# Performance work log

Hardware: AMD Instinct MI355X
Metric: run time of the kernel (lower is better)

Reference implementation:

```python
import jax, jax.numpy as jnp
import numpy as np

B, N, S, K = 8, 16384, 1024, 32
C_STEM, C_PATCH, PE_DIM = 64, 128, 24
RADIUS = 0.2
NUM_BANDS = PE_DIM // 6  # 4 freq bands, sin+cos per xyz axis -> 3*2*4 = 24


def setup_inputs() -> dict:
    key = jax.random.key(0)
    ks = jax.random.split(key, 6)
    xyz = jax.random.uniform(ks[0], (B, N, 3), dtype=jnp.float32)
    point_feature = jax.random.normal(ks[1], (B, N, C_STEM), dtype=jnp.float32)
    patch_center = jax.random.uniform(ks[2], (B, S, 3), dtype=jnp.float32)
    in_dim = C_STEM + 3 + PE_DIM  # grouped_feature + relative_xyz + pos-enc
    w1 = jax.random.normal(ks[3], (in_dim, C_PATCH), dtype=jnp.float32) / np.sqrt(in_dim)
    b1 = jnp.zeros((C_PATCH,), dtype=jnp.float32)
    w2 = jax.random.normal(ks[4], (C_PATCH, C_PATCH), dtype=jnp.float32) / np.sqrt(C_PATCH)
    b2 = jnp.zeros((C_PATCH,), dtype=jnp.float32)
    return dict(xyz=xyz, point_feature=point_feature, patch_center=patch_center,
                w1=w1, b1=b1, w2=w2, b2=b2)


def query_ball_point(radius, nsample, xyz, new_xyz):
    # Standard PointNet++ ball query. xyz:[B,N,3], new_xyz:[B,S,3] -> idx:[B,S,K]
    n = xyz.shape[1]
    sqrdists = jnp.sum((new_xyz[:, :, None, :] - xyz[:, None, :, :]) ** 2, axis=-1)  # [B,S,N]
    gi = jnp.where(sqrdists > radius * radius, n,
                   jnp.arange(n, dtype=jnp.int32)[None, None, :])
    gi = jnp.sort(gi, axis=-1)[:, :, :nsample]           # first K in-ball indices
    first = gi[:, :, :1]
    gi = jnp.where(gi == n, first, gi)                   # pad misses with first hit
    return jnp.minimum(gi, n - 1)


def index_points(points, idx):
    # points:[B,N,C], idx:[B,S,K] -> [B,S,K,C]
    b = points.shape[0]
    return points[jnp.arange(b)[:, None, None], idx]


def pos_encode(rel):
    # NeRF-style sinusoidal encoding of relative xyz: [...,3] -> [...,PE_DIM]
    freqs = (2.0 ** jnp.arange(NUM_BANDS, dtype=jnp.float32)) * jnp.pi
    ang = rel[..., None] * freqs                          # [...,3,NB]
    enc = jnp.concatenate([jnp.sin(ang), jnp.cos(ang)], axis=-1)  # [...,3,2NB]
    return enc.reshape(rel.shape[:-1] + (PE_DIM,))


def reference(xyz, point_feature, patch_center, w1, b1, w2, b2):
    neighbor_idx = query_ball_point(RADIUS, K, xyz, patch_center)   # [B,S,K]
    grouped_xyz = index_points(xyz, neighbor_idx)                    # [B,S,K,3]
    grouped_feature = index_points(point_feature, neighbor_idx)      # [B,S,K,C_STEM]
    relative_xyz = grouped_xyz - patch_center[:, :, None, :]
    relative_position = pos_encode(relative_xyz)                     # [B,S,K,PE_DIM]
    grouped_input = jnp.concatenate(
        (grouped_feature, relative_xyz, relative_position), axis=-1)  # [B,S,K,91]
    h = jax.nn.relu(grouped_input @ w1 + b1)   # PointMLP 1 (shared per-point MLP)
    h = h @ w2 + b2                            # PointMLP 2 (no activation)
    patch_feature = jnp.max(h, axis=2)         # max-pool over K neighbors -> [B,S,C_PATCH]
    return (patch_feature, neighbor_idx)
```

## Files before the change

kernel.cpp:

```cpp
#include <hip/hip_runtime.h>
#include <hip/hip_bf16.h>

#define B_ 8
#define N_ 16384
#define S_ 1024
#define K_ 32
#define CSTEM 64
#define CPATCH 128
#define INDIM 91
#define LDA 104
#define LDH 136

typedef __attribute__((ext_vector_type(8))) short short8v;
typedef __attribute__((ext_vector_type(4))) float f32x4;

static __device__ __forceinline__ unsigned short f2bf(float f) {
  union { float f; unsigned int u; } v; v.f = f;
  return (unsigned short)((v.u + 0x7FFFu + ((v.u >> 16) & 1u)) >> 16);
}

__global__ __launch_bounds__(256) void pack_weights(
    const float* __restrict__ w1, const float* __restrict__ w2,
    unsigned short* __restrict__ w1p, unsigned short* __restrict__ w2p)
{
  const int id = blockIdx.x * 256 + threadIdx.x;
  if (id < 3 * 8 * 64) {
    const int l = id & 63, ct = (id >> 6) & 7, ks = id >> 9;
    const int col = 16 * ct + (l & 15);
    const int kb = 32 * ks + (l >> 4) * 8;
    unsigned short v[8];
    #pragma unroll
    for (int j = 0; j < 8; ++j) {
      const int k = kb + j;
      v[j] = (k < INDIM) ? f2bf(w1[k * CPATCH + col]) : (unsigned short)0;
    }
    *(short8v*)&w1p[(size_t)id * 8] = *(const short8v*)v;
  } else if (id < 3 * 8 * 64 + 4 * 8 * 64) {
    const int id2 = id - 3 * 8 * 64;
    const int l = id2 & 63, ct = (id2 >> 6) & 7, ks = id2 >> 9;
    const int col = 16 * ct + (l & 15);
    const int kb = 32 * ks + (l >> 4) * 8;
    unsigned short v[8];
    #pragma unroll
    for (int j = 0; j < 8; ++j) v[j] = f2bf(w2[(kb + j) * CPATCH + col]);
    *(short8v*)&w2p[(size_t)id2 * 8] = *(const short8v*)v;
  }
}

__global__ __launch_bounds__(256, 6) void ball_query_kernel(
    const float* __restrict__ xyz, const float* __restrict__ pc,
    float* __restrict__ idx_out)
{
  const int w    = threadIdx.x >> 6;
  const int lane = threadIdx.x & 63;
  const int bs   = blockIdx.x * 4 + w;
  const int b    = bs >> 10;

  const float* __restrict__ xb = xyz + (size_t)b * N_ * 3;
  const double cx = (double)pc[bs * 3 + 0];
  const double cy = (double)pc[bs * 3 + 1];
  const double cz = (double)pc[bs * 3 + 2];
  const double rr = 0.2 * 0.2;

  __shared__ int fidx[4][K_];

  const unsigned long long lower = (1ull << lane) - 1ull;
  int found = 0;
  for (int base = 0; base < N_; base += 256) {
    const int i0 = base + lane * 4;
    const float4 p0 = *(const float4*)&xb[i0 * 3 + 0];
    const float4 p1 = *(const float4*)&xb[i0 * 3 + 4];
    const float4 p2 = *(const float4*)&xb[i0 * 3 + 8];

    double dx, dy, dz;
    dx = (double)p0.x - cx; dy = (double)p0.y - cy; dz = (double)p0.z - cz;
    const bool in0 = (dx * dx + dy * dy + dz * dz) <= rr;
    dx = (double)p0.w - cx; dy = (double)p1.x - cy; dz = (double)p1.y - cz;
    const bool in1 = (dx * dx + dy * dy + dz * dz) <= rr;
    dx = (double)p1.z - cx; dy = (double)p1.w - cy; dz = (double)p2.x - cz;
    const bool in2 = (dx * dx + dy * dy + dz * dz) <= rr;
    dx = (double)p2.y - cx; dy = (double)p2.z - cy; dz = (double)p2.w - cz;
    const bool in3 = (dx * dx + dy * dy + dz * dz) <= rr;

    const unsigned long long b0 = __ballot(in0);
    const unsigned long long b1 = __ballot(in1);
    const unsigned long long b2 = __ballot(in2);
    const unsigned long long b3 = __ballot(in3);

    int p = found + __popcll(b0 & lower) + __popcll(b1 & lower)
                  + __popcll(b2 & lower) + __popcll(b3 & lower);
    if (in0) { if (p < K_) fidx[w][p] = i0 + 0; ++p; }
    if (in1) { if (p < K_) fidx[w][p] = i0 + 1; ++p; }
    if (in2) { if (p < K_) fidx[w][p] = i0 + 2; ++p; }
    if (in3) { if (p < K_) fidx[w][p] = i0 + 3; }

    found += __popcll(b0) + __popcll(b1) + __popcll(b2) + __popcll(b3);
    if (found >= K_) break;
  }
  __threadfence_block();
  if (lane < K_) {
    const int fill = (found == 0) ? (N_ - 1) : fidx[w][0];
    const int v = (lane < found) ? fidx[w][lane] : fill;
    idx_out[(size_t)bs * K_ + lane] = (float)v;
  }
}

__global__ __launch_bounds__(256) void patch_mlp_mfma(
    const float* __restrict__ xyz, const float* __restrict__ pf,
    const float* __restrict__ pc,
    const unsigned short* __restrict__ w1p, const float* __restrict__ b1,
    const unsigned short* __restrict__ w2p, const float* __restrict__ b2,
    const float* __restrict__ idx_f, float* __restrict__ out)
{
  const int bs   = blockIdx.x;
  const int b    = bs >> 10;
  const int tid  = threadIdx.x;
  const int lane = tid & 63;
  const int w    = tid >> 6;

  __shared__ int sidx[K_];
  __shared__ float scen[3];
  __shared__ __align__(16) unsigned short As[K_][LDA];
  __shared__ __align__(16) unsigned short Hs[K_][LDH];

  if (tid < K_) sidx[tid] = (int)idx_f[(size_t)bs * K_ + tid];
  if (tid < 3)  scen[tid] = pc[bs * 3 + tid];
  __syncthreads();

  const float* __restrict__ pfb = pf  + (size_t)b * N_ * CSTEM;
  const float* __restrict__ xb  = xyz + (size_t)b * N_ * 3;

  {
    const int row = tid >> 3, sub = tid & 7;
    const int r = sidx[row];
    const float4 f0 = *(const float4*)&pfb[(size_t)r * CSTEM + sub * 8];
    const float4 f1 = *(const float4*)&pfb[(size_t)r * CSTEM + sub * 8 + 4];
    unsigned short v[8];
    v[0] = f2bf(f0.x); v[1] = f2bf(f0.y); v[2] = f2bf(f0.z); v[3] = f2bf(f0.w);
    v[4] = f2bf(f1.x); v[5] = f2bf(f1.y); v[6] = f2bf(f1.z); v[7] = f2bf(f1.w);
    *(short8v*)&As[row][sub * 8] = *(const short8v*)v;
  }
  {
    const int row = tid & 31, j = tid >> 5;
    const int r = sidx[row];
    float rel[3];
    rel[0] = xb[r * 3 + 0] - scen[0];
    rel[1] = xb[r * 3 + 1] - scen[1];
    rel[2] = xb[r * 3 + 2] - scen[2];
    #pragma unroll
    for (int cc = 0; cc < 4; ++cc) {
      const int c = 64 + 4 * j + cc;
      float val;
      if (c < 67) val = rel[c - 64];
      else if (c < 91) {
        const int q = c - 67, d = q >> 3, rbit = q & 7, band = rbit & 3;
        const float ang = rel[d] * ((float)(1 << band) * 3.14159265358979323846f);
        val = (rbit < 4) ? sinf(ang) : cosf(ang);
      } else val = 0.f;
      As[row][c] = f2bf(val);
    }
  }
  __syncthreads();

  f32x4 acc[2][2] = {};
  #pragma unroll
  for (int ks = 0; ks < 3; ++ks) {
    const int k0 = ks * 32 + (lane >> 4) * 8;
    const short8v a0 = *(const short8v*)&As[(lane & 15)][k0];
    const short8v a1 = *(const short8v*)&As[16 + (lane & 15)][k0];
    const short8v bA = *(const short8v*)&w1p[((size_t)(ks * 8 + 2 * w) * 64 + lane) * 8];
    const short8v bB = *(const short8v*)&w1p[((size_t)(ks * 8 + 2 * w + 1) * 64 + lane) * 8];
    acc[0][0] = __builtin_amdgcn_mfma_f32_16x16x32_bf16(a0, bA, acc[0][0], 0, 0, 0);
    acc[0][1] = __builtin_amdgcn_mfma_f32_16x16x32_bf16(a0, bB, acc[0][1], 0, 0, 0);
    acc[1][0] = __builtin_amdgcn_mfma_f32_16x16x32_bf16(a1, bA, acc[1][0], 0, 0, 0);
    acc[1][1] = __builtin_amdgcn_mfma_f32_16x16x32_bf16(a1, bB, acc[1][1], 0, 0, 0);
  }
  const float bias1[2] = { b1[32 * w + (lane & 15)], b1[32 * w + 16 + (lane & 15)] };
  #pragma unroll
  for (int rt = 0; rt < 2; ++rt)
    #pragma unroll
    for (int t = 0; t < 2; ++t)
      #pragma unroll
      for (int reg = 0; reg < 4; ++reg) {
        const float h = fmaxf(acc[rt][t][reg] + bias1[t], 0.f);
        const int row = 16 * rt + (lane >> 4) * 4 + reg;
        const int col = 32 * w + 16 * t + (lane & 15);
        Hs[row][col] = f2bf(h);
      }
  __syncthreads();

  f32x4 acc2[2][2] = {};
  #pragma unroll
  for (int ks = 0; ks < 4; ++ks) {
    const int k0 = ks * 32 + (lane >> 4) * 8;
    const short8v a0 = *(const short8v*)&Hs[(lane & 15)][k0];
    const short8v a1 = *(const short8v*)&Hs[16 + (lane & 15)][k0];
    const short8v bA = *(const short8v*)&w2p[((size_t)(ks * 8 + 2 * w) * 64 + lane) * 8];
    const short8v bB = *(const short8v*)&w2p[((size_t)(ks * 8 + 2 * w + 1) * 64 + lane) * 8];
    acc2[0][0] = __builtin_amdgcn_mfma_f32_16x16x32_bf16(a0, bA, acc2[0][0], 0, 0, 0);
    acc2[0][1] = __builtin_amdgcn_mfma_f32_16x16x32_bf16(a0, bB, acc2[0][1], 0, 0, 0);
    acc2[1][0] = __builtin_amdgcn_mfma_f32_16x16x32_bf16(a1, bA, acc2[1][0], 0, 0, 0);
    acc2[1][1] = __builtin_amdgcn_mfma_f32_16x16x32_bf16(a1, bB, acc2[1][1], 0, 0, 0);
  }
  float m0 = -3.4e38f, m1 = -3.4e38f;
  #pragma unroll
  for (int rt = 0; rt < 2; ++rt)
    #pragma unroll
    for (int reg = 0; reg < 4; ++reg) {
      m0 = fmaxf(m0, acc2[rt][0][reg]);
      m1 = fmaxf(m1, acc2[rt][1][reg]);
    }
  m0 += b2[32 * w + (lane & 15)];
  m1 += b2[32 * w + 16 + (lane & 15)];
  m0 = fmaxf(m0, __shfl_xor(m0, 16));
  m0 = fmaxf(m0, __shfl_xor(m0, 32));
  m1 = fmaxf(m1, __shfl_xor(m1, 16));
  m1 = fmaxf(m1, __shfl_xor(m1, 32));
  if (lane < 16) {
    out[(size_t)bs * CPATCH + 32 * w + lane]      = m0;
    out[(size_t)bs * CPATCH + 32 * w + 16 + lane] = m1;
  }
}

extern "C" void kernel_launch(void* const* d_in, const int* in_sizes, int n_in,
                              void* d_out, int out_size, void* d_ws, size_t ws_size,
                              hipStream_t stream) {
  const float* xyz = (const float*)d_in[0];
  const float* pf  = (const float*)d_in[1];
  const float* pc  = (const float*)d_in[2];
  const float* w1  = (const float*)d_in[3];
  const float* b1  = (const float*)d_in[4];
  const float* w2  = (const float*)d_in[5];
  const float* b2  = (const float*)d_in[6];

  float* out     = (float*)d_out;
  float* idx_out = out + (size_t)B_ * S_ * CPATCH;

  unsigned short* w1p = (unsigned short*)d_ws;
  unsigned short* w2p = w1p + 96 * 128;

  pack_weights<<<14, 256, 0, stream>>>(w1, w2, w1p, w2p);
  ball_query_kernel<<<B_ * S_ / 4, 256, 0, stream>>>(xyz, pc, idx_out);
  patch_mlp_mfma<<<B_ * S_, 256, 0, stream>>>(xyz, pf, pc, w1p, b1, w2p, b2,
                                              idx_out, out);
}
```

Before: 53.90 us.

## Process several patches per MLP block with register-resident weights; prefetch ball-query points

The MLP kernel now handles four patches per block. Each wave loads its W1/W2 MFMA fragments and biases into registers once and reuses them across all four patches, instead of reloading them from global memory for every patch. The ball-query loop is software-pipelined so the next 256-point chunk of xyz is loaded while the current chunk is tested. In exchange the MLP kernel uses more registers and launches fewer blocks, and each patch iteration still runs serially with block-wide barriers, so there is less latency hiding.

```diff
diff --git a/kernel.cpp b/kernel.cpp
--- a/kernel.cpp
+++ b/kernel.cpp
@@ -10,6 +10,7 @@
 #define INDIM 91
 #define LDA 104
 #define LDH 136
+#define PPB 4
 
 typedef __attribute__((ext_vector_type(8))) short short8v;
 typedef __attribute__((ext_vector_type(4))) float f32x4;
@@ -65,21 +66,30 @@
   __shared__ int fidx[4][K_];
 
   const unsigned long long lower = (1ull << lane) - 1ull;
+  const int lo3 = lane * 12;
   int found = 0;
-  for (int base = 0; base < N_; base += 256) {
+  int base = 0;
+
+  float4 c0 = *(const float4*)&xb[lo3 + 0];
+  float4 c1 = *(const float4*)&xb[lo3 + 4];
+  float4 c2 = *(const float4*)&xb[lo3 + 8];
+
+  for (;;) {
+    const bool last = (base + 256 >= N_);
+    const int pb = last ? base : base + 256;
+    const float4 n0 = *(const float4*)&xb[pb * 3 + lo3 + 0];
+    const float4 n1 = *(const float4*)&xb[pb * 3 + lo3 + 4];
+    const float4 n2 = *(const float4*)&xb[pb * 3 + lo3 + 8];
+
     const int i0 = base + lane * 4;
-    const float4 p0 = *(const float4*)&xb[i0 * 3 + 0];
-    const float4 p1 = *(const float4*)&xb[i0 * 3 + 4];
-    const float4 p2 = *(const float4*)&xb[i0 * 3 + 8];
-
     double dx, dy, dz;
-    dx = (double)p0.x - cx; dy = (double)p0.y - cy; dz = (double)p0.z - cz;
+    dx = (double)c0.x - cx; dy = (double)c0.y - cy; dz = (double)c0.z - cz;
     const bool in0 = (dx * dx + dy * dy + dz * dz) <= rr;
-    dx = (double)p0.w - cx; dy = (double)p1.x - cy; dz = (double)p1.y - cz;
+    dx = (double)c0.w - cx; dy = (double)c1.x - cy; dz = (double)c1.y - cz;
     const bool in1 = (dx * dx + dy * dy + dz * dz) <= rr;
-    dx = (double)p1.z - cx; dy = (double)p1.w - cy; dz = (double)p2.x - cz;
+    dx = (double)c1.z - cx; dy = (double)c1.w - cy; dz = (double)c2.x - cz;
     const bool in2 = (dx * dx + dy * dy + dz * dz) <= rr;
-    dx = (double)p2.y - cx; dy = (double)p2.z - cy; dz = (double)p2.w - cz;
+    dx = (double)c2.y - cx; dy = (double)c2.z - cy; dz = (double)c2.w - cz;
     const bool in3 = (dx * dx + dy * dy + dz * dz) <= rr;
 
     const unsigned long long b0 = __ballot(in0);
@@ -95,7 +105,9 @@
     if (in3) { if (p < K_) fidx[w][p] = i0 + 3; }
 
     found += __popcll(b0) + __popcll(b1) + __popcll(b2) + __popcll(b3);
-    if (found >= K_) break;
+    if (found >= K_ || last) break;
+    base += 256;
+    c0 = n0; c1 = n1; c2 = n2;
   }
   __threadfence_block();
   if (lane < K_) {
@@ -105,15 +117,13 @@
   }
 }
 
-__global__ __launch_bounds__(256) void patch_mlp_mfma(
+__global__ __launch_bounds__(256, 2) void patch_mlp_mfma(
     const float* __restrict__ xyz, const float* __restrict__ pf,
     const float* __restrict__ pc,
     const unsigned short* __restrict__ w1p, const float* __restrict__ b1,
     const unsigned short* __restrict__ w2p, const float* __restrict__ b2,
     const float* __restrict__ idx_f, float* __restrict__ out)
 {
-  const int bs   = blockIdx.x;
-  const int b    = bs >> 10;
   const int tid  = threadIdx.x;
   const int lane = tid & 63;
   const int w    = tid >> 6;
@@ -123,102 +133,117 @@
   __shared__ __align__(16) unsigned short As[K_][LDA];
   __shared__ __align__(16) unsigned short Hs[K_][LDH];
 
-  if (tid < K_) sidx[tid] = (int)idx_f[(size_t)bs * K_ + tid];
-  if (tid < 3)  scen[tid] = pc[bs * 3 + tid];
-  __syncthreads();
-
-  const float* __restrict__ pfb = pf  + (size_t)b * N_ * CSTEM;
-  const float* __restrict__ xb  = xyz + (size_t)b * N_ * 3;
-
-  {
-    const int row = tid >> 3, sub = tid & 7;
-    const int r = sidx[row];
-    const float4 f0 = *(const float4*)&pfb[(size_t)r * CSTEM + sub * 8];
-    const float4 f1 = *(const float4*)&pfb[(size_t)r * CSTEM + sub * 8 + 4];
-    unsigned short v[8];
-    v[0] = f2bf(f0.x); v[1] = f2bf(f0.y); v[2] = f2bf(f0.z); v[3] = f2bf(f0.w);
-    v[4] = f2bf(f1.x); v[5] = f2bf(f1.y); v[6] = f2bf(f1.z); v[7] = f2bf(f1.w);
-    *(short8v*)&As[row][sub * 8] = *(const short8v*)v;
-  }
-  {
-    const int row = tid & 31, j = tid >> 5;
-    const int r = sidx[row];
-    float rel[3];
-    rel[0] = xb[r * 3 + 0] - scen[0];
-    rel[1] = xb[r * 3 + 1] - scen[1];
-    rel[2] = xb[r * 3 + 2] - scen[2];
-    #pragma unroll
-    for (int cc = 0; cc < 4; ++cc) {
-      const int c = 64 + 4 * j + cc;
-      float val;
-      if (c < 67) val = rel[c - 64];
-      else if (c < 91) {
-        const int q = c - 67, d = q >> 3, rbit = q & 7, band = rbit & 3;
-        const float ang = rel[d] * ((float)(1 << band) * 3.14159265358979323846f);
-        val = (rbit < 4) ? sinf(ang) : cosf(ang);
-      } else val = 0.f;
-      As[row][c] = f2bf(val);
-    }
-  }
-  __syncthreads();
-
-  f32x4 acc[2][2] = {};
+  short8v w1f[3][2], w2f[4][2];
   #pragma unroll
-  for (int ks = 0; ks < 3; ++ks) {
-    const int k0 = ks * 32 + (lane >> 4) * 8;
-    const short8v a0 = *(const short8v*)&As[(lane & 15)][k0];
-    const short8v a1 = *(const short8v*)&As[16 + (lane & 15)][k0];
-    const short8v bA = *(const short8v*)&w1p[((size_t)(ks * 8 + 2 * w) * 64 + lane) * 8];
-    const short8v bB = *(const short8v*)&w1p[((size_t)(ks * 8 + 2 * w + 1) * 64 + lane) * 8];
-    acc[0][0] = __builtin_amdgcn_mfma_f32_16x16x32_bf16(a0, bA, acc[0][0], 0, 0, 0);
-    acc[0][1] = __builtin_amdgcn_mfma_f32_16x16x32_bf16(a0, bB, acc[0][1], 0, 0, 0);
-    acc[1][0] = __builtin_amdgcn_mfma_f32_16x16x32_bf16(a1, bA, acc[1][0], 0, 0, 0);
-    acc[1][1] = __builtin_amdgcn_mfma_f32_16x16x32_bf16(a1, bB, acc[1][1], 0, 0, 0);
-  }
+  for (int ks = 0; ks < 3; ++ks)
+    #pragma unroll
+    for (int t = 0; t < 2; ++t)
+      w1f[ks][t] = *(const short8v*)&w1p[((size_t)(ks * 8 + 2 * w + t) * 64 + lane) * 8];
+  #pragma unroll
+  for (int ks = 0; ks < 4; ++ks)
+    #pragma unroll
+    for (int t = 0; t < 2; ++t)
+      w2f[ks][t] = *(const short8v*)&w2p[((size_t)(ks * 8 + 2 * w + t) * 64 + lane) * 8];
+
   const float bias1[2] = { b1[32 * w + (lane & 15)], b1[32 * w + 16 + (lane & 15)] };
-  #pragma unroll
-  for (int rt = 0; rt < 2; ++rt)
-    #pragma unroll
-    for (int t = 0; t < 2; ++t)
+  const float bias2[2] = { b2[32 * w + (lane & 15)], b2[32 * w + 16 + (lane & 15)] };
+
+  for (int p = 0; p < PPB; ++p) {
+    const int bs = blockIdx.x * PPB + p;
+    const int b  = bs >> 10;
+    const float* __restrict__ pfb = pf  + (size_t)b * N_ * CSTEM;
+    const float* __restrict__ xb  = xyz + (size_t)b * N_ * 3;
+
+    if (tid < K_) sidx[tid] = (int)idx_f[(size_t)bs * K_ + tid];
+    if (tid < 3)  scen[tid] = pc[bs * 3 + tid];
+    __syncthreads();
+
+    {
+      const int row = tid >> 3, sub = tid & 7;
+      const int r = sidx[row];
+      const float4 f0 = *(const float4*)&pfb[(size_t)r * CSTEM + sub * 8];
+      const float4 f1 = *(const float4*)&pfb[(size_t)r * CSTEM + sub * 8 + 4];
+      unsigned short v[8];
+      v[0] = f2bf(f0.x); v[1] = f2bf(f0.y); v[2] = f2bf(f0.z); v[3] = f2bf(f0.w);
+      v[4] = f2bf(f1.x); v[5] = f2bf(f1.y); v[6] = f2bf(f1.z); v[7] = f2bf(f1.w);
+      *(short8v*)&As[row][sub * 8] = *(const short8v*)v;
+    }
+    {
+      const int row = tid & 31, j = tid >> 5;
+      const int r = sidx[row];
+      float rel[3];
+      rel[0] = xb[r * 3 + 0] - scen[0];
+      rel[1] = xb[r * 3 + 1] - scen[1];
+      rel[2] = xb[r * 3 + 2] - scen[2];
+      #pragma unroll
+      for (int cc = 0; cc < 4; ++cc) {
+        const int c = 64 + 4 * j + cc;
+        float val;
+        if (c < 67) val = rel[c - 64];
+        else if (c < 91) {
+          const int q = c - 67, d = q >> 3, rbit = q & 7, band = rbit & 3;
+          const float ang = rel[d] * ((float)(1 << band) * 3.14159265358979323846f);
+          val = (rbit < 4) ? sinf(ang) : cosf(ang);
+        } else val = 0.f;
+        As[row][c] = f2bf(val);
+      }
+    }
+    __syncthreads();
+
+    f32x4 acc[2][2] = {};
+    #pragma unroll
+    for (int ks = 0; ks < 3; ++ks) {
+      const int k0 = ks * 32 + (lane >> 4) * 8;
+      const short8v a0 = *(const short8v*)&As[(lane & 15)][k0];
+      const short8v a1 = *(const short8v*)&As[16 + (lane & 15)][k0];
+      acc[0][0] = __builtin_amdgcn_mfma_f32_16x16x32_bf16(a0, w1f[ks][0], acc[0][0], 0, 0, 0);
+      acc[0][1] = __builtin_amdgcn_mfma_f32_16x16x32_bf16(a0, w1f[ks][1], acc[0][1], 0, 0, 0);
+      acc[1][0] = __builtin_amdgcn_mfma_f32_16x16x32_bf16(a1, w1f[ks][0], acc[1][0], 0, 0, 0);
+      acc[1][1] = __builtin_amdgcn_mfma_f32_16x16x32_bf16(a1, w1f[ks][1], acc[1][1], 0, 0, 0);
+    }
+    #pragma unroll
+    for (int rt = 0; rt < 2; ++rt)
+      #pragma unroll
+      for (int t = 0; t < 2; ++t)
+        #pragma unroll
+        for (int reg = 0; reg < 4; ++reg) {
+          const float h = fmaxf(acc[rt][t][reg] + bias1[t], 0.f);
+          const int row = 16 * rt + (lane >> 4) * 4 + reg;
+          const int col = 32 * w + 16 * t + (lane & 15);
+          Hs[row][col] = f2bf(h);
+        }
+    __syncthreads();
+
+    f32x4 acc2[2][2] = {};
+    #pragma unroll
+    for (int ks = 0; ks < 4; ++ks) {
+      const int k0 = ks * 32 + (lane >> 4) * 8;
+      const short8v a0 = *(const short8v*)&Hs[(lane & 15)][k0];
+      const short8v a1 = *(const short8v*)&Hs[16 + (lane & 15)][k0];
+      acc2[0][0] = __builtin_amdgcn_mfma_f32_16x16x32_bf16(a0, w2f[ks][0], acc2[0][0], 0, 0, 0);
+      acc2[0][1] = __builtin_amdgcn_mfma_f32_16x16x32_bf16(a0, w2f[ks][1], acc2[0][1], 0, 0, 0);
+      acc2[1][0] = __builtin_amdgcn_mfma_f32_16x16x32_bf16(a1, w2f[ks][0], acc2[1][0], 0, 0, 0);
+      acc2[1][1] = __builtin_amdgcn_mfma_f32_16x16x32_bf16(a1, w2f[ks][1], acc2[1][1], 0, 0, 0);
+    }
+    float m0 = -3.4e38f, m1 = -3.4e38f;
+    #pragma unroll
+    for (int rt = 0; rt < 2; ++rt)
       #pragma unroll
       for (int reg = 0; reg < 4; ++reg) {
-        const float h = fmaxf(acc[rt][t][reg] + bias1[t], 0.f);
-        const int row = 16 * rt + (lane >> 4) * 4 + reg;
-        const int col = 32 * w + 16 * t + (lane & 15);
-        Hs[row][col] = f2bf(h);
+        m0 = fmaxf(m0, acc2[rt][0][reg]);
+        m1 = fmaxf(m1, acc2[rt][1][reg]);
       }
-  __syncthreads();
-
-  f32x4 acc2[2][2] = {};
-  #pragma unroll
-  for (int ks = 0; ks < 4; ++ks) {
-    const int k0 = ks * 32 + (lane >> 4) * 8;
-    const short8v a0 = *(const short8v*)&Hs[(lane & 15)][k0];
-    const short8v a1 = *(const short8v*)&Hs[16 + (lane & 15)][k0];
-    const short8v bA = *(const short8v*)&w2p[((size_t)(ks * 8 + 2 * w) * 64 + lane) * 8];
-    const short8v bB = *(const short8v*)&w2p[((size_t)(ks * 8 + 2 * w + 1) * 64 + lane) * 8];
-    acc2[0][0] = __builtin_amdgcn_mfma_f32_16x16x32_bf16(a0, bA, acc2[0][0], 0, 0, 0);
-    acc2[0][1] = __builtin_amdgcn_mfma_f32_16x16x32_bf16(a0, bB, acc2[0][1], 0, 0, 0);
-    acc2[1][0] = __builtin_amdgcn_mfma_f32_16x16x32_bf16(a1, bA, acc2[1][0], 0, 0, 0);
-    acc2[1][1] = __builtin_amdgcn_mfma_f32_16x16x32_bf16(a1, bB, acc2[1][1], 0, 0, 0);
-  }
-  float m0 = -3.4e38f, m1 = -3.4e38f;
-  #pragma unroll
-  for (int rt = 0; rt < 2; ++rt)
-    #pragma unroll
-    for (int reg = 0; reg < 4; ++reg) {
-      m0 = fmaxf(m0, acc2[rt][0][reg]);
-      m1 = fmaxf(m1, acc2[rt][1][reg]);
-    }
-  m0 += b2[32 * w + (lane & 15)];
-  m1 += b2[32 * w + 16 + (lane & 15)];
-  m0 = fmaxf(m0, __shfl_xor(m0, 16));
-  m0 = fmaxf(m0, __shfl_xor(m0, 32));
-  m1 = fmaxf(m1, __shfl_xor(m1, 16));
-  m1 = fmaxf(m1, __shfl_xor(m1, 32));
-  if (lane < 16) {
-    out[(size_t)bs * CPATCH + 32 * w + lane]      = m0;
-    out[(size_t)bs * CPATCH + 32 * w + 16 + lane] = m1;
+    m0 += bias2[0];
+    m1 += bias2[1];
+    m0 = fmaxf(m0, __shfl_xor(m0, 16));
+    m0 = fmaxf(m0, __shfl_xor(m0, 32));
+    m1 = fmaxf(m1, __shfl_xor(m1, 16));
+    m1 = fmaxf(m1, __shfl_xor(m1, 32));
+    if (lane < 16) {
+      out[(size_t)bs * CPATCH + 32 * w + lane]      = m0;
+      out[(size_t)bs * CPATCH + 32 * w + 16 + lane] = m1;
+    }
+    __syncthreads();
   }
 }
 
@@ -241,6 +266,6 @@
 
   pack_weights<<<14, 256, 0, stream>>>(w1, w2, w1p, w2p);
   ball_query_kernel<<<B_ * S_ / 4, 256, 0, stream>>>(xyz, pc, idx_out);
-  patch_mlp_mfma<<<B_ * S_, 256, 0, stream>>>(xyz, pf, pc, w1p, b1, w2p, b2,
-                                              idx_out, out);
-}
+  patch_mlp_mfma<<<B_ * S_ / PPB, 256, 0, stream>>>(xyz, pf, pc, w1p, b1, w2p, b2,
+                                                    idx_out, out);
+}
```

Result: no change. 54.04 us (+0.3%).
